# Performance work log

Hardware: AMD Instinct MI355X
Metric: run time of the kernel (lower is better)

## Reference

```python
import jax, jax.numpy as jnp
import numpy as np

NUM_CLASSES = 4      # config.class_num (malaria stages)
N = 2048             # total nodes = source + target samples
S = 1024             # source_length
FEAT_IN = 25088      # VGG19 include_top=False -> 7*7*512 flattened
D_FC = 512           # Dense(512)
D_G1 = 512           # config.features_dim (GCNConv1 out)
D_G2 = 256           # config.GCN_hidderlayer_dim_num (GCNConv2 out)


def setup_inputs() -> dict:
    key = jax.random.key(0)
    ks = jax.random.split(key, 8)
    sc = lambda fan_in: np.float32(1.0 / np.sqrt(fan_in))
    return {
        "x": jax.random.normal(ks[0], (N, FEAT_IN), jnp.float32),
        "W_fc": jax.random.normal(ks[1], (FEAT_IN, D_FC), jnp.float32) * sc(FEAT_IN),
        "b_fc": jnp.zeros((D_FC,), jnp.float32),
        "W_g1": jax.random.normal(ks[2], (D_FC, D_G1), jnp.float32) * sc(D_FC),
        "b_g1": jnp.zeros((D_G1,), jnp.float32),
        "W_g2": jax.random.normal(ks[3], (D_G1, D_G2), jnp.float32) * sc(D_G1),
        "b_g2": jnp.zeros((D_G2,), jnp.float32),
        "source_labels": jax.random.randint(ks[4], (S,), 0, NUM_CLASSES),
        "source_length": S,
    }


def reference(x, W_fc, b_fc, W_g1, b_g1, W_g2, b_g2, source_labels, source_length):
    # fc after (omitted frozen) VGG19 backbone + flatten
    feats = x @ W_fc + b_fc                                   # [N, 512]

    # get_centers: per-class SUM of source features (no averaging, faithful)
    src = feats[:source_length]                               # [S, 512]
    centers = jax.ops.segment_sum(src, source_labels, num_segments=NUM_CLASSES)  # [C, 512]

    # per-target euclidean distance to each centroid + argmin
    # (argmin of squared distance == argmin of euclidean distance)
    tgt = feats[source_length:]                               # [T, 512]
    d2 = (jnp.sum(tgt * tgt, axis=1, keepdims=True)
          - 2.0 * (tgt @ centers.T)
          + jnp.sum(centers * centers, axis=1)[None, :])      # [T, C]
    target_labels = jnp.argmin(d2, axis=1)                    # [T] int

    # label-cluster graph: edge iff same label; source block forced to identity
    all_labels = jnp.concatenate([source_labels.astype(jnp.int32),
                                  target_labels.astype(jnp.int32)])
    adj = (all_labels[:, None] == all_labels[None, :]).astype(feats.dtype)  # [N, N]
    adj = adj.at[:source_length, :source_length].set(
        jnp.eye(source_length, dtype=feats.dtype))

    # add_self_loops(value=1) then symmetric gcn_filter D^-1/2 A D^-1/2
    A = adj + jnp.eye(N, dtype=feats.dtype)
    dinv = jax.lax.rsqrt(jnp.sum(A, axis=1))                  # [N]
    A_norm = dinv[:, None] * A * dinv[None, :]                # [N, N]

    # two GCN layers (spektral GCNConv: A_norm @ (X @ W) + b) with relu
    h = jax.nn.relu(A_norm @ (feats @ W_g1) + b_g1)           # [N, 512]
    h = jax.nn.relu(A_norm @ (h @ W_g2) + b_g2)               # [N, 256]
    return (h, A_norm, feats)
```

## Files before the change

### kernel.cpp

```cpp
#include <hip/hip_runtime.h>

#define NROWS 2048
#define SLEN  1024
#define FEAT  25088
#define DFC   512
#define DG1   512
#define DG2   256
#define CSPLIT 128

typedef __attribute__((ext_vector_type(8))) short short8;
typedef __attribute__((ext_vector_type(4))) float f32x4;

__device__ __forceinline__ unsigned short bfbits(float f) {
  unsigned int u = __float_as_uint(f);
  u += 0x7fffu + ((u >> 16) & 1u);
  return (unsigned short)(u >> 16);
}

__device__ __forceinline__ unsigned int cvtpk(float lo, float hi) {
  unsigned int r;
  asm("v_cvt_pk_bf16_f32 %0, %1, %2" : "=v"(r) : "v"(lo), "v"(hi));
  return r;
}

__device__ __forceinline__ void load_lds16(const void* g, void* l) {
  __builtin_amdgcn_global_load_lds(
      (const __attribute__((address_space(1))) unsigned int*)g,
      (__attribute__((address_space(3))) unsigned int*)l, 16, 0, 0);
}

__global__ void transpose_cvt_k(const float* __restrict__ src, unsigned short* __restrict__ dst,
                                int K, int Ncol) {
  __shared__ float tile[64][65];
  int kb = blockIdx.x * 64, nb = blockIdx.y * 64;
  int tx = threadIdx.x & 63, ty = threadIdx.x >> 6;
  #pragma unroll
  for (int i = ty; i < 64; i += 4)
    tile[i][tx] = src[(size_t)(kb + i) * Ncol + (nb + tx)];
  __syncthreads();
  #pragma unroll
  for (int i = ty; i < 64; i += 4)
    dst[(size_t)(nb + i) * K + (kb + tx)] = bfbits(tile[tx][i]);
}

__global__ __launch_bounds__(512, 2) void gemm_fc_k(const float* __restrict__ A,
    const unsigned short* __restrict__ BT, float* __restrict__ Cacc, int ksteps) {
  __shared__ unsigned short Al[2][256 * 32];
  __shared__ unsigned short Bl[2][256 * 32];
  const int K = FEAT;
  int tid = threadIdx.x;
  int m0 = (blockIdx.x >> 1) * 256;
  int n0 = (blockIdx.x & 1) * 256;
  int kbase = blockIdx.y * ksteps * 32;
  int wid = tid >> 6, lane = tid & 63;
  int wm = wid >> 1, wn = wid & 1;
  int lrow = lane & 15, lko = lane >> 4;

  f32x4 acc[4][8];
  #pragma unroll
  for (int i = 0; i < 4; i++)
    #pragma unroll
    for (int j = 0; j < 8; j++) acc[i][j] = (f32x4){0.f, 0.f, 0.f, 0.f};

  float4 pa[4];

  auto loadA_regs = [&](int k0) {
    #pragma unroll
    for (int j = 0; j < 2; j++) {
      int ch = tid + j * 512;
      int r = ch >> 2, c = ch & 3;
      const float* g = A + (size_t)(m0 + r) * K + k0 + c * 8;
      pa[2 * j]     = *reinterpret_cast<const float4*>(g);
      pa[2 * j + 1] = *reinterpret_cast<const float4*>(g + 4);
    }
  };
  auto cvtWriteA = [&](int buf) {
    #pragma unroll
    for (int j = 0; j < 2; j++) {
      int ch = tid + j * 512;
      int r = ch >> 2, c = ch & 3;
      int p = c ^ (r & 3);
      int4 o;
      o.x = (int)cvtpk(pa[2 * j].x,     pa[2 * j].y);
      o.y = (int)cvtpk(pa[2 * j].z,     pa[2 * j].w);
      o.z = (int)cvtpk(pa[2 * j + 1].x, pa[2 * j + 1].y);
      o.w = (int)cvtpk(pa[2 * j + 1].z, pa[2 * j + 1].w);
      *reinterpret_cast<int4*>((char*)Al[buf] + r * 64 + p * 16) = o;
    }
  };
  auto stageB = [&](int buf, int k0) {
    #pragma unroll
    for (int j = 0; j < 2; j++) {
      int chb = wid * 128 + j * 64;
      int ch = chb + lane;
      int r = ch >> 2, c = (ch & 3) ^ (r & 3);
      load_lds16(BT + (size_t)(n0 + r) * K + k0 + c * 8, (char*)Bl[buf] + chb * 16);
    }
  };

  loadA_regs(kbase);
  stageB(0, kbase);
  cvtWriteA(0);
  loadA_regs(kbase + 32);
  stageB(1, kbase + 32);
  asm volatile("s_waitcnt vmcnt(6)" ::: "memory");
  asm volatile("s_waitcnt lgkmcnt(0)" ::: "memory");
  __builtin_amdgcn_s_barrier();
  __builtin_amdgcn_sched_barrier(0);

  int cur = 0;
  for (int t = 0; t < ksteps; ++t) {
    bool more1 = (t + 1 < ksteps), more2 = (t + 2 < ksteps);
    if (more1) cvtWriteA(cur ^ 1);
    short8 af[4], bf8[8];
    #pragma unroll
    for (int mi = 0; mi < 4; mi++) {
      int R = wm * 64 + mi * 16 + lrow;
      int p = lko ^ (R & 3);
      af[mi] = *reinterpret_cast<const short8*>((char*)Al[cur] + R * 64 + p * 16);
    }
    #pragma unroll
    for (int ni = 0; ni < 8; ni++) {
      int R = wn * 128 + ni * 16 + lrow;
      int p = lko ^ (R & 3);
      bf8[ni] = *reinterpret_cast<const short8*>((char*)Bl[cur] + R * 64 + p * 16);
    }
    if (more2) loadA_regs(kbase + (t + 2) * 32);
    asm volatile("s_waitcnt lgkmcnt(0)" ::: "memory");
    __builtin_amdgcn_s_barrier();
    __builtin_amdgcn_sched_barrier(0);
    if (more2) stageB(cur, kbase + (t + 2) * 32);
    #pragma unroll
    for (int mi = 0; mi < 4; mi++)
      #pragma unroll
      for (int ni = 0; ni < 8; ni++)
        acc[mi][ni] = __builtin_amdgcn_mfma_f32_16x16x32_bf16(af[mi], bf8[ni], acc[mi][ni], 0, 0, 0);
    if (more1) {
      if (more2) { asm volatile("s_waitcnt vmcnt(6)" ::: "memory"); }
      else       { asm volatile("s_waitcnt vmcnt(0)" ::: "memory"); }
      __builtin_amdgcn_sched_barrier(0);
    }
    cur ^= 1;
  }

  #pragma unroll
  for (int mi = 0; mi < 4; mi++)
    #pragma unroll
    for (int ni = 0; ni < 8; ni++)
      #pragma unroll
      for (int r = 0; r < 4; r++) {
        int row = m0 + wm * 64 + mi * 16 + lko * 4 + r;
        int col = n0 + wn * 128 + ni * 16 + lrow;
        atomicAdd(&Cacc[(size_t)row * DFC + col], acc[mi][ni][r]);
      }
}

__global__ __launch_bounds__(256) void gemm_l_k(const unsigned short* __restrict__ A,
    const unsigned short* __restrict__ BT, float* __restrict__ Cacc,
    int K, int Ncols, int tiles_n, int ksteps) {
  __shared__ unsigned short Al[2][128 * 64];
  __shared__ unsigned short Bl[2][128 * 64];
  int tid = threadIdx.x;
  int m0 = (blockIdx.x / tiles_n) * 128;
  int n0 = (blockIdx.x % tiles_n) * 128;
  int kbase = blockIdx.y * ksteps * 64;
  int wid = tid >> 6, lane = tid & 63;
  int wm = wid >> 1, wn = wid & 1;
  int lrow = lane & 15, lko = lane >> 4;

  f32x4 acc[4][4];
  #pragma unroll
  for (int i = 0; i < 4; i++)
    #pragma unroll
    for (int j = 0; j < 4; j++) acc[i][j] = (f32x4){0.f, 0.f, 0.f, 0.f};

  auto stage = [&](unsigned short (*L)[128 * 64], const unsigned short* G, int buf, int k0) {
    #pragma unroll
    for (int j = 0; j < 4; j++) {
      int chb = j * 256 + wid * 64;
      int ch = chb + lane;
      int r = ch >> 3, c = (ch & 7) ^ (r & 7);
      load_lds16(G + (size_t)r * K + k0 + c * 8, (char*)L[buf] + chb * 16);
    }
  };

  stage(Al, A + (size_t)m0 * K, 0, kbase);
  stage(Bl, BT + (size_t)n0 * K, 0, kbase);
  __syncthreads();

  int cur = 0;
  for (int t = 0; t < ksteps; ++t) {
    bool more = (t + 1 < ksteps);
    if (more) {
      stage(Al, A + (size_t)m0 * K, cur ^ 1, kbase + (t + 1) * 64);
      stage(Bl, BT + (size_t)n0 * K, cur ^ 1, kbase + (t + 1) * 64);
    }
    #pragma unroll
    for (int kk = 0; kk < 2; kk++) {
      short8 af[4], bfv[4];
      #pragma unroll
      for (int mi = 0; mi < 4; mi++) {
        int R = wm * 64 + mi * 16 + lrow;
        int slot = ((kk << 2) | lko) ^ (lrow & 7);
        af[mi] = *reinterpret_cast<const short8*>((char*)Al[cur] + R * 128 + slot * 16);
      }
      #pragma unroll
      for (int ni = 0; ni < 4; ni++) {
        int R = wn * 64 + ni * 16 + lrow;
        int slot = ((kk << 2) | lko) ^ (lrow & 7);
        bfv[ni] = *reinterpret_cast<const short8*>((char*)Bl[cur] + R * 128 + slot * 16);
      }
      #pragma unroll
      for (int mi = 0; mi < 4; mi++)
        #pragma unroll
        for (int ni = 0; ni < 4; ni++)
          acc[mi][ni] = __builtin_amdgcn_mfma_f32_16x16x32_bf16(af[mi], bfv[ni], acc[mi][ni], 0, 0, 0);
    }
    __syncthreads();
    cur ^= 1;
  }
  #pragma unroll
  for (int mi = 0; mi < 4; mi++)
    #pragma unroll
    for (int ni = 0; ni < 4; ni++)
      #pragma unroll
      for (int r = 0; r < 4; r++) {
        int row = m0 + wm * 64 + mi * 16 + lko * 4 + r;
        int col = n0 + wn * 64 + ni * 16 + lrow;
        atomicAdd(&Cacc[(size_t)row * Ncols + col], acc[mi][ni][r]);
      }
}

__global__ void feats_fin_k(const float* __restrict__ facc, const float* __restrict__ bfc,
                            float* __restrict__ outf, unsigned short* __restrict__ outbf) {
  int i = blockIdx.y;
  int n = blockIdx.x * 256 + threadIdx.x;
  float v = facc[(size_t)i * DFC + n] + bfc[n];
  outf[(size_t)i * DFC + n] = v;
  outbf[(size_t)i * DFC + n] = bfbits(v);
}

__global__ void seg_sum_part_k(const float* __restrict__ x, const int* __restrict__ slab,
                               float* __restrict__ sxp) {
  int k4 = blockIdx.x * 256 + threadIdx.x;
  if (k4 >= FEAT / 4) return;
  int k = k4 * 4;
  int i0 = blockIdx.y * 64, i1 = i0 + 64;
  float4 a0 = {0,0,0,0}, a1 = {0,0,0,0}, a2 = {0,0,0,0}, a3 = {0,0,0,0};
  #pragma unroll 4
  for (int i = i0; i < i1; i++) {
    float4 v = *reinterpret_cast<const float4*>(x + (size_t)i * FEAT + k);
    int c = slab[i];
    float m0 = (c == 0) ? 1.f : 0.f, m1 = (c == 1) ? 1.f : 0.f;
    float m2 = (c == 2) ? 1.f : 0.f, m3 = (c == 3) ? 1.f : 0.f;
    a0.x += m0 * v.x; a0.y += m0 * v.y; a0.z += m0 * v.z; a0.w += m0 * v.w;
    a1.x += m1 * v.x; a1.y += m1 * v.y; a1.z += m1 * v.z; a1.w += m1 * v.w;
    a2.x += m2 * v.x; a2.y += m2 * v.y; a2.z += m2 * v.z; a2.w += m2 * v.w;
    a3.x += m3 * v.x; a3.y += m3 * v.y; a3.z += m3 * v.z; a3.w += m3 * v.w;
  }
  size_t base = (size_t)blockIdx.y * 4 * FEAT;
  *reinterpret_cast<float4*>(sxp + base + 0 * FEAT + k) = a0;
  *reinterpret_cast<float4*>(sxp + base + 1 * FEAT + k) = a1;
  *reinterpret_cast<float4*>(sxp + base + 2 * FEAT + k) = a2;
  *reinterpret_cast<float4*>(sxp + base + 3 * FEAT + k) = a3;
}

__global__ void seg_sum_reduce_k(const float* __restrict__ sxp, float* __restrict__ sx) {
  int k4 = blockIdx.x * 256 + threadIdx.x;
  if (k4 >= FEAT / 4) return;
  int k = k4 * 4;
  int c = blockIdx.y;
  double s0 = 0, s1 = 0, s2 = 0, s3 = 0;
  #pragma unroll
  for (int p = 0; p < 16; p++) {
    float4 v = *reinterpret_cast<const float4*>(sxp + ((size_t)p * 4 + c) * FEAT + k);
    s0 += (double)v.x; s1 += (double)v.y; s2 += (double)v.z; s3 += (double)v.w;
  }
  float4 r; r.x = (float)s0; r.y = (float)s1; r.z = (float)s2; r.w = (float)s3;
  *reinterpret_cast<float4*>(sx + (size_t)c * FEAT + k) = r;
}

__global__ void count_src_k(const int* __restrict__ slab, int* __restrict__ cnt) {
  __shared__ int c[4];
  if (threadIdx.x < 4) c[threadIdx.x] = 0;
  __syncthreads();
  for (int i = threadIdx.x; i < SLEN; i += 256) atomicAdd(&c[slab[i]], 1);
  __syncthreads();
  if (threadIdx.x < 4) cnt[threadIdx.x] = c[threadIdx.x];
}

__global__ void centers_part_k(const float* __restrict__ sx, const float* __restrict__ W,
                               double* __restrict__ cpart) {
  int n = blockIdx.x * 64 + (threadIdx.x & 63);
  int cc = threadIdx.x >> 6;
  int kb = blockIdx.y * (FEAT / CSPLIT), ke = kb + FEAT / CSPLIT;
  const float* sr = sx + (size_t)cc * FEAT;
  double acc = 0.0;
  #pragma unroll 4
  for (int k = kb; k < ke; k++)
    acc += (double)sr[k] * (double)W[(size_t)k * DFC + n];
  cpart[((size_t)blockIdx.y * 4 + cc) * DFC + n] = acc;
}

__global__ void centers_reduce_k(const double* __restrict__ cpart, const float* __restrict__ bfc,
                                 const int* __restrict__ cntsrc, float* __restrict__ Cent) {
  int idx = blockIdx.x * 256 + threadIdx.x;
  int cc = idx >> 9, n = idx & 511;
  double s = 0.0;
  #pragma unroll 4
  for (int p = 0; p < CSPLIT; p++) s += cpart[((size_t)p * 4 + cc) * DFC + n];
  Cent[idx] = (float)(s + (double)cntsrc[cc] * (double)bfc[n]);
}

__global__ void wc_k(const float* __restrict__ W, const float* __restrict__ Cent,
                     float* __restrict__ wc) {
  __shared__ float cs[4 * DFC];
  for (int i = threadIdx.x; i < 4 * DFC; i += 256) cs[i] = Cent[i];
  __syncthreads();
  int k = blockIdx.x * 256 + threadIdx.x;
  if (k >= FEAT) return;
  const float* wr = W + (size_t)k * DFC;
  double a0 = 0, a1 = 0, a2 = 0, a3 = 0;
  #pragma unroll 2
  for (int n = 0; n < DFC; n += 4) {
    float4 w4 = *reinterpret_cast<const float4*>(wr + n);
    a0 += (double)w4.x * cs[0 * DFC + n] + (double)w4.y * cs[0 * DFC + n + 1]
        + (double)w4.z * cs[0 * DFC + n + 2] + (double)w4.w * cs[0 * DFC + n + 3];
    a1 += (double)w4.x * cs[1 * DFC + n] + (double)w4.y * cs[1 * DFC + n + 1]
        + (double)w4.z * cs[1 * DFC + n + 2] + (double)w4.w * cs[1 * DFC + n + 3];
    a2 += (double)w4.x * cs[2 * DFC + n] + (double)w4.y * cs[2 * DFC + n + 1]
        + (double)w4.z * cs[2 * DFC + n + 2] + (double)w4.w * cs[2 * DFC + n + 3];
    a3 += (double)w4.x * cs[3 * DFC + n] + (double)w4.y * cs[3 * DFC + n + 1]
        + (double)w4.z * cs[3 * DFC + n + 2] + (double)w4.w * cs[3 * DFC + n + 3];
  }
  float4 r; r.x = (float)a0; r.y = (float)a1; r.z = (float)a2; r.w = (float)a3;
  *reinterpret_cast<float4*>(wc + 4 * (size_t)k) = r;
}

__global__ void kj_k(const float* __restrict__ Cent, const float* __restrict__ bfc,
                     float* __restrict__ Kj) {
  int j = threadIdx.x >> 6, lane = threadIdx.x & 63;
  float cn = 0.f, bc = 0.f;
  for (int n = lane; n < DFC; n += 64) {
    float c = Cent[j * DFC + n];
    cn += c * c; bc += bfc[n] * c;
  }
  #pragma unroll
  for (int m = 32; m >= 1; m >>= 1) { cn += __shfl_xor(cn, m); bc += __shfl_xor(bc, m); }
  if (lane == 0) Kj[j] = cn - 2.f * bc;
}

__global__ void d2_labels_k(const float* __restrict__ x, const float* __restrict__ wc,
                            const float* __restrict__ Kj, int* __restrict__ tlab) {
  int row = blockIdx.x;
  int tid = threadIdx.x;
  const float* xr = x + (size_t)(SLEN + row) * FEAT;
  double a0 = 0, a1 = 0, a2 = 0, a3 = 0;
  #pragma unroll 2
  for (int k = tid; k < FEAT; k += 256) {
    float xv = xr[k];
    float4 w4 = *reinterpret_cast<const float4*>(wc + 4 * (size_t)k);
    a0 += (double)xv * w4.x; a1 += (double)xv * w4.y;
    a2 += (double)xv * w4.z; a3 += (double)xv * w4.w;
  }
  #pragma unroll
  for (int m = 32; m >= 1; m >>= 1) {
    a0 += __shfl_xor(a0, m); a1 += __shfl_xor(a1, m);
    a2 += __shfl_xor(a2, m); a3 += __shfl_xor(a3, m);
  }
  __shared__ double s[4][4];
  int wid = tid >> 6, lane = tid & 63;
  if (lane == 0) { s[wid][0] = a0; s[wid][1] = a1; s[wid][2] = a2; s[wid][3] = a3; }
  __syncthreads();
  if (tid == 0) {
    double t0 = s[0][0] + s[1][0] + s[2][0] + s[3][0];
    double t1 = s[0][1] + s[1][1] + s[2][1] + s[3][1];
    double t2 = s[0][2] + s[1][2] + s[2][2] + s[3][2];
    double t3 = s[0][3] + s[1][3] + s[2][3] + s[3][3];
    double s0 = (double)Kj[0] - 2.0 * t0;
    double s1 = (double)Kj[1] - 2.0 * t1;
    double s2 = (double)Kj[2] - 2.0 * t2;
    double s3 = (double)Kj[3] - 2.0 * t3;
    int bi = 0; double b = s0;
    if (s1 < b) { b = s1; bi = 1; }
    if (s2 < b) { b = s2; bi = 2; }
    if (s3 < b) { b = s3; bi = 3; }
    tlab[row] = bi;
  }
}

__global__ void finalize_labels_k(const int* __restrict__ slab, const int* __restrict__ tlab,
                                  const int* __restrict__ cntsrc, int* __restrict__ alllab,
                                  float* __restrict__ dinv) {
  __shared__ int ct[4];
  if (threadIdx.x < 4) ct[threadIdx.x] = 0;
  __syncthreads();
  for (int i = threadIdx.x; i < SLEN; i += 256) atomicAdd(&ct[tlab[i]], 1);
  __syncthreads();
  for (int i = threadIdx.x; i < NROWS; i += 256) {
    int lab = (i < SLEN) ? slab[i] : tlab[i - SLEN];
    alllab[i] = lab;
    float rs = (i < SLEN) ? (2.f + (float)ct[lab])
                          : (1.f + (float)cntsrc[lab] + (float)ct[lab]);
    dinv[i] = 1.f / sqrtf(rs);
  }
}

__global__ void anorm_k(const int* __restrict__ alllab, const float* __restrict__ dinv,
                        float* __restrict__ Aout) {
  int i = blockIdx.y;
  int j0 = (blockIdx.x * 256 + threadIdx.x) * 4;
  int li = alllab[i];
  float di = dinv[i];
  int4 lj = *reinterpret_cast<const int4*>(alllab + j0);
  float4 dj = *reinterpret_cast<const float4*>(dinv + j0);
  int jj[4] = {lj.x, lj.y, lj.z, lj.w};
  float dd[4] = {dj.x, dj.y, dj.z, dj.w};
  float4 o;
  float* op = &o.x;
  #pragma unroll
  for (int e = 0; e < 4; e++) {
    int j = j0 + e;
    float v;
    if (i == j) v = 2.f * di * dd[e];
    else if (i < SLEN && j < SLEN) v = 0.f;
    else v = (li == jj[e]) ? di * dd[e] : 0.f;
    op[e] = v;
  }
  *reinterpret_cast<float4*>(Aout + (size_t)i * NROWS + j0) = o;
}

__global__ void reduce_st_k(const float* __restrict__ Xacc, const int* __restrict__ alllab,
                            const float* __restrict__ dinv, float* __restrict__ ST, int D) {
  int n = blockIdx.x * 256 + threadIdx.x;
  int i0 = blockIdx.y * 32, i1 = i0 + 32;
  float s[4] = {0, 0, 0, 0}, tt[4] = {0, 0, 0, 0};
  for (int i = i0; i < i1; ++i) {
    float v = dinv[i] * Xacc[(size_t)i * D + n];
    int lab = alllab[i];
    bool src = i < SLEN;
    #pragma unroll
    for (int c = 0; c < 4; c++) {
      s[c]  += (src && lab == c) ? v : 0.f;
      tt[c] += (!src && lab == c) ? v : 0.f;
    }
  }
  #pragma unroll
  for (int c = 0; c < 4; c++) {
    atomicAdd(&ST[c * D + n], s[c]);
    atomicAdd(&ST[(4 + c) * D + n], tt[c]);
  }
}

__global__ void apply_prop_k(const float* __restrict__ Xacc, const float* __restrict__ ST,
                             const int* __restrict__ alllab, const float* __restrict__ dinv,
                             const float* __restrict__ bias, float* __restrict__ outf,
                             unsigned short* __restrict__ outbf, int D) {
  int i = blockIdx.y;
  int n = blockIdx.x * 256 + threadIdx.x;
  float dv = dinv[i];
  int lab = alllab[i];
  float xv = Xacc[(size_t)i * D + n];
  float z;
  if (i < SLEN) z = dv * (2.f * dv * xv + ST[(4 + lab) * D + n]);
  else          z = dv * (ST[lab * D + n] + ST[(4 + lab) * D + n] + dv * xv);
  z += bias[n];
  z = fmaxf(z, 0.f);
  if (outf)  outf[(size_t)i * D + n] = z;
  if (outbf) outbf[(size_t)i * D + n] = bfbits(z);
}

extern "C" void kernel_launch(void* const* d_in, const int* in_sizes, int n_in,
                              void* d_out, int out_size, void* d_ws, size_t ws_size,
                              hipStream_t stream) {
  const float* x    = (const float*)d_in[0];
  const float* Wfc  = (const float*)d_in[1];
  const float* bfc  = (const float*)d_in[2];
  const float* Wg1  = (const float*)d_in[3];
  const float* bg1  = (const float*)d_in[4];
  const float* Wg2  = (const float*)d_in[5];
  const float* bg2  = (const float*)d_in[6];
  const int*   slab = (const int*)d_in[7];

  float* out = (float*)d_out;
  float* out_h = out;
  float* out_A = out + 524288;
  float* out_f = out + 4718592;

  char* w = (char*)d_ws;
  unsigned short* wT   = (unsigned short*)(w);
  unsigned short* g1T  = (unsigned short*)(w + 25690112);
  unsigned short* g2T  = (unsigned short*)(w + 26214400);
  float* facc          = (float*)(w + 26476544);
  unsigned short* fbf  = (unsigned short*)(w + 30670848);
  float* x1acc         = (float*)(w + 32768000);
  unsigned short* h1bf = (unsigned short*)(w + 36962304);
  float* x2acc         = (float*)(w + 39059456);
  float* sx            = (float*)(w + 41156608);
  float* Cent          = (float*)(w + 41623552);
  float* wc            = (float*)(w + 41631744);
  float* Kj            = (float*)(w + 42033152);
  int*   tlab          = (int*)(w + 42033216);
  int*   alllab        = (int*)(w + 42037312);
  float* dinv          = (float*)(w + 42045504);
  int*   cntsrc        = (int*)(w + 42053696);
  float* ST1           = (float*)(w + 42053760);
  float* ST2           = (float*)(w + 42070144);

  float*  sxp     = (float*)(w + 32768000);
  double* cpart_d = (double*)(w + 39059456);

  hipMemsetAsync(facc,  0, (size_t)NROWS * DFC * 4, stream);
  hipMemsetAsync(ST1,   0, 8 * DG1 * 4, stream);
  hipMemsetAsync(ST2,   0, 8 * DG2 * 4, stream);

  transpose_cvt_k<<<dim3(FEAT / 64, DFC / 64), 256, 0, stream>>>(Wfc, wT, FEAT, DFC);
  transpose_cvt_k<<<dim3(DFC / 64, DG1 / 64), 256, 0, stream>>>(Wg1, g1T, DFC, DG1);
  transpose_cvt_k<<<dim3(DG1 / 64, DG2 / 64), 256, 0, stream>>>(Wg2, g2T, DG1, DG2);

  gemm_fc_k<<<dim3(16, 16), 512, 0, stream>>>(x, wT, facc, 49);
  feats_fin_k<<<dim3(DFC / 256, NROWS), 256, 0, stream>>>(facc, bfc, out_f, fbf);

  seg_sum_part_k<<<dim3(25, 16), 256, 0, stream>>>(x, slab, sxp);
  seg_sum_reduce_k<<<dim3(25, 4), 256, 0, stream>>>(sxp, sx);
  count_src_k<<<1, 256, 0, stream>>>(slab, cntsrc);
  centers_part_k<<<dim3(DFC / 64, CSPLIT), 256, 0, stream>>>(sx, Wfc, cpart_d);
  centers_reduce_k<<<dim3(4 * DFC / 256), 256, 0, stream>>>(cpart_d, bfc, cntsrc, Cent);
  wc_k<<<dim3(FEAT / 256), 256, 0, stream>>>(Wfc, Cent, wc);
  kj_k<<<1, 256, 0, stream>>>(Cent, bfc, Kj);
  d2_labels_k<<<dim3(NROWS - SLEN), 256, 0, stream>>>(x, wc, Kj, tlab);
  finalize_labels_k<<<1, 256, 0, stream>>>(slab, tlab, cntsrc, alllab, dinv);

  anorm_k<<<dim3(NROWS / 1024, NROWS), 256, 0, stream>>>(alllab, dinv, out_A);

  hipMemsetAsync(x1acc, 0, (size_t)NROWS * DG1 * 4, stream);
  gemm_l_k<<<dim3(16 * 4, 4), 256, 0, stream>>>(fbf, g1T, x1acc, DFC, DG1, 4, 2);
  reduce_st_k<<<dim3(DG1 / 256, 64), 256, 0, stream>>>(x1acc, alllab, dinv, ST1, DG1);
  apply_prop_k<<<dim3(DG1 / 256, NROWS), 256, 0, stream>>>(x1acc, ST1, alllab, dinv, bg1,
                                                           nullptr, h1bf, DG1);

  hipMemsetAsync(x2acc, 0, (size_t)NROWS * DG2 * 4, stream);
  gemm_l_k<<<dim3(16 * 2, 8), 256, 0, stream>>>(h1bf, g2T, x2acc, DG1, DG2, 2, 1);
  reduce_st_k<<<dim3(DG2 / 256, 64), 256, 0, stream>>>(x2acc, alllab, dinv, ST2, DG2);
  apply_prop_k<<<dim3(DG2 / 256, NROWS), 256, 0, stream>>>(x2acc, ST2, alllab, dinv, bg2,
                                                           out_h, nullptr, DG2);

  (void)in_sizes; (void)n_in; (void)out_size; (void)ws_size;
}
```

Baseline: 356.3 us.

## Triple-buffer LDS and deepen prefetch pipeline in FC GEMM

The fc GEMM kernel moves from double to triple buffering of the A and B LDS tiles. A and B loads are now issued three k-steps ahead, using two ping-pong register sets for the fp32 A prefetch, and the vmcnt waits are reworked to match. The LDS swizzle also changes to XOR with (row>>1)&3 to reduce bank conflicts. The aim is to hide more global-memory latency in this bandwidth-heavy 25088-deep reduction, at the cost of more LDS (96KB per block at 2 blocks/CU) and more registers, which may lower occupancy.

```diff
diff --git a/kernel.cpp b/kernel.cpp
--- a/kernel.cpp
+++ b/kernel.cpp
@@ -45,8 +45,8 @@
 
 __global__ __launch_bounds__(512, 2) void gemm_fc_k(const float* __restrict__ A,
     const unsigned short* __restrict__ BT, float* __restrict__ Cacc, int ksteps) {
-  __shared__ unsigned short Al[2][256 * 32];
-  __shared__ unsigned short Bl[2][256 * 32];
+  __shared__ unsigned short Al[3][256 * 32];
+  __shared__ unsigned short Bl[3][256 * 32];
   const int K = FEAT;
   int tid = threadIdx.x;
   int m0 = (blockIdx.x >> 1) * 256;
@@ -62,9 +62,9 @@
     #pragma unroll
     for (int j = 0; j < 8; j++) acc[i][j] = (f32x4){0.f, 0.f, 0.f, 0.f};
 
-  float4 pa[4];
-
-  auto loadA_regs = [&](int k0) {
+  float4 pa0[4], pa1[4];
+
+  auto loadA = [&](float4 (&pa)[4], int k0) {
     #pragma unroll
     for (int j = 0; j < 2; j++) {
       int ch = tid + j * 512;
@@ -74,73 +74,77 @@
       pa[2 * j + 1] = *reinterpret_cast<const float4*>(g + 4);
     }
   };
-  auto cvtWriteA = [&](int buf) {
+  auto cvtA = [&](float4 (&pa)[4], unsigned short* L) {
     #pragma unroll
     for (int j = 0; j < 2; j++) {
       int ch = tid + j * 512;
       int r = ch >> 2, c = ch & 3;
-      int p = c ^ (r & 3);
+      int p = c ^ ((r >> 1) & 3);
       int4 o;
       o.x = (int)cvtpk(pa[2 * j].x,     pa[2 * j].y);
       o.y = (int)cvtpk(pa[2 * j].z,     pa[2 * j].w);
       o.z = (int)cvtpk(pa[2 * j + 1].x, pa[2 * j + 1].y);
       o.w = (int)cvtpk(pa[2 * j + 1].z, pa[2 * j + 1].w);
-      *reinterpret_cast<int4*>((char*)Al[buf] + r * 64 + p * 16) = o;
+      *reinterpret_cast<int4*>((char*)L + r * 64 + p * 16) = o;
     }
   };
-  auto stageB = [&](int buf, int k0) {
+  auto stB = [&](unsigned short* L, int k0) {
     #pragma unroll
     for (int j = 0; j < 2; j++) {
       int chb = wid * 128 + j * 64;
       int ch = chb + lane;
-      int r = ch >> 2, c = (ch & 3) ^ (r & 3);
-      load_lds16(BT + (size_t)(n0 + r) * K + k0 + c * 8, (char*)Bl[buf] + chb * 16);
+      int r = ch >> 2, p = ch & 3;
+      int c = p ^ ((r >> 1) & 3);
+      load_lds16(BT + (size_t)(n0 + r) * K + k0 + c * 8, (char*)L + chb * 16);
     }
   };
 
-  loadA_regs(kbase);
-  stageB(0, kbase);
-  cvtWriteA(0);
-  loadA_regs(kbase + 32);
-  stageB(1, kbase + 32);
-  asm volatile("s_waitcnt vmcnt(6)" ::: "memory");
+  stB(Bl[0], kbase);
+  loadA(pa0, kbase);
+  loadA(pa1, kbase + 32);
+  cvtA(pa0, Al[0]);
+  stB(Bl[1], kbase + 32);
+  loadA(pa0, kbase + 64);
+  stB(Bl[2], kbase + 64);
   asm volatile("s_waitcnt lgkmcnt(0)" ::: "memory");
   __builtin_amdgcn_s_barrier();
   __builtin_amdgcn_sched_barrier(0);
 
   int cur = 0;
-  for (int t = 0; t < ksteps; ++t) {
-    bool more1 = (t + 1 < ksteps), more2 = (t + 2 < ksteps);
-    if (more1) cvtWriteA(cur ^ 1);
+  auto step = [&](int t, float4 (&pa)[4]) {
+    int nxt = (cur == 2) ? 0 : cur + 1;
+    if (t + 1 < ksteps) cvtA(pa, Al[nxt]);
     short8 af[4], bf8[8];
     #pragma unroll
     for (int mi = 0; mi < 4; mi++) {
       int R = wm * 64 + mi * 16 + lrow;
-      int p = lko ^ (R & 3);
+      int p = lko ^ ((R >> 1) & 3);
       af[mi] = *reinterpret_cast<const short8*>((char*)Al[cur] + R * 64 + p * 16);
     }
     #pragma unroll
     for (int ni = 0; ni < 8; ni++) {
       int R = wn * 128 + ni * 16 + lrow;
-      int p = lko ^ (R & 3);
+      int p = lko ^ ((R >> 1) & 3);
       bf8[ni] = *reinterpret_cast<const short8*>((char*)Bl[cur] + R * 64 + p * 16);
     }
-    if (more2) loadA_regs(kbase + (t + 2) * 32);
+    if (t + 3 < ksteps) loadA(pa, kbase + (t + 3) * 32);
+    if (t < ksteps - 4) { asm volatile("s_waitcnt vmcnt(10)" ::: "memory"); }
+    else                { asm volatile("s_waitcnt vmcnt(0)"  ::: "memory"); }
     asm volatile("s_waitcnt lgkmcnt(0)" ::: "memory");
     __builtin_amdgcn_s_barrier();
     __builtin_amdgcn_sched_barrier(0);
-    if (more2) stageB(cur, kbase + (t + 2) * 32);
+    if (t + 3 < ksteps) stB(Bl[cur], kbase + (t + 3) * 32);
     #pragma unroll
     for (int mi = 0; mi < 4; mi++)
       #pragma unroll
       for (int ni = 0; ni < 8; ni++)
         acc[mi][ni] = __builtin_amdgcn_mfma_f32_16x16x32_bf16(af[mi], bf8[ni], acc[mi][ni], 0, 0, 0);
-    if (more1) {
-      if (more2) { asm volatile("s_waitcnt vmcnt(6)" ::: "memory"); }
-      else       { asm volatile("s_waitcnt vmcnt(0)" ::: "memory"); }
-      __builtin_amdgcn_sched_barrier(0);
-    }
-    cur ^= 1;
+    cur = nxt;
+  };
+
+  for (int t0 = 0; t0 < ksteps; t0 += 2) {
+    step(t0, pa1);
+    if (t0 + 1 < ksteps) step(t0 + 1, pa0);
   }
 
   #pragma unroll
```

Result: no change. 357.6 us (+0.4%).

## Shrink fc GEMM tiles to 128x128 with simple single-buffered loop

Applied to the files above, without the earlier changes.

Replaces the 256x256-tile, 512-thread, register-prefetched double-buffered fc GEMM with a 128x128-tile, 256-thread kernel that loads, converts and stages each k-step synchronously. This raises block count and allows more blocks per CU so occupancy can hide latency instead of explicit pipelining. It also changes the LDS swizzle pattern. The trade-off is that the fp32 input matrix is re-read twice as often and prefetch overlap is lost.

```diff
diff --git a/kernel.cpp b/kernel.cpp
--- a/kernel.cpp
+++ b/kernel.cpp
@@ -43,114 +43,81 @@
     dst[(size_t)(nb + i) * K + (kb + tx)] = bfbits(tile[tx][i]);
 }
 
-__global__ __launch_bounds__(512, 2) void gemm_fc_k(const float* __restrict__ A,
+__global__ __launch_bounds__(256, 4) void gemm_fc_k(const float* __restrict__ A,
     const unsigned short* __restrict__ BT, float* __restrict__ Cacc, int ksteps) {
-  __shared__ unsigned short Al[2][256 * 32];
-  __shared__ unsigned short Bl[2][256 * 32];
+  __shared__ unsigned short Al[128 * 32];
+  __shared__ unsigned short Bl[128 * 32];
   const int K = FEAT;
   int tid = threadIdx.x;
-  int m0 = (blockIdx.x >> 1) * 256;
-  int n0 = (blockIdx.x & 1) * 256;
+  int m0 = (blockIdx.x >> 2) * 128;
+  int n0 = (blockIdx.x & 3) * 128;
   int kbase = blockIdx.y * ksteps * 32;
   int wid = tid >> 6, lane = tid & 63;
   int wm = wid >> 1, wn = wid & 1;
   int lrow = lane & 15, lko = lane >> 4;
 
-  f32x4 acc[4][8];
+  int chA0 = tid, rA0 = chA0 >> 2, cA0 = chA0 & 3, pA0 = cA0 ^ ((rA0 >> 1) & 3);
+  int chA1 = tid + 256, rA1 = chA1 >> 2, cA1 = chA1 & 3, pA1 = cA1 ^ ((rA1 >> 1) & 3);
+  int chB0 = wid * 128 + lane;
+  int chB1 = wid * 128 + 64 + lane;
+  int rB0 = chB0 >> 2, cB0 = (chB0 & 3) ^ ((rB0 >> 1) & 3);
+  int rB1 = chB1 >> 2, cB1 = (chB1 & 3) ^ ((rB1 >> 1) & 3);
+  const float* gA0 = A + (size_t)(m0 + rA0) * K + cA0 * 8;
+  const float* gA1 = A + (size_t)(m0 + rA1) * K + cA1 * 8;
+  const unsigned short* gB0 = BT + (size_t)(n0 + rB0) * K + cB0 * 8;
+  const unsigned short* gB1 = BT + (size_t)(n0 + rB1) * K + cB1 * 8;
+
+  f32x4 acc[4][4];
   #pragma unroll
   for (int i = 0; i < 4; i++)
     #pragma unroll
-    for (int j = 0; j < 8; j++) acc[i][j] = (f32x4){0.f, 0.f, 0.f, 0.f};
-
-  float4 pa[4];
-
-  auto loadA_regs = [&](int k0) {
-    #pragma unroll
-    for (int j = 0; j < 2; j++) {
-      int ch = tid + j * 512;
-      int r = ch >> 2, c = ch & 3;
-      const float* g = A + (size_t)(m0 + r) * K + k0 + c * 8;
-      pa[2 * j]     = *reinterpret_cast<const float4*>(g);
-      pa[2 * j + 1] = *reinterpret_cast<const float4*>(g + 4);
-    }
-  };
-  auto cvtWriteA = [&](int buf) {
-    #pragma unroll
-    for (int j = 0; j < 2; j++) {
-      int ch = tid + j * 512;
-      int r = ch >> 2, c = ch & 3;
-      int p = c ^ (r & 3);
-      int4 o;
-      o.x = (int)cvtpk(pa[2 * j].x,     pa[2 * j].y);
-      o.y = (int)cvtpk(pa[2 * j].z,     pa[2 * j].w);
-      o.z = (int)cvtpk(pa[2 * j + 1].x, pa[2 * j + 1].y);
-      o.w = (int)cvtpk(pa[2 * j + 1].z, pa[2 * j + 1].w);
-      *reinterpret_cast<int4*>((char*)Al[buf] + r * 64 + p * 16) = o;
-    }
-  };
-  auto stageB = [&](int buf, int k0) {
-    #pragma unroll
-    for (int j = 0; j < 2; j++) {
-      int chb = wid * 128 + j * 64;
-      int ch = chb + lane;
-      int r = ch >> 2, c = (ch & 3) ^ (r & 3);
-      load_lds16(BT + (size_t)(n0 + r) * K + k0 + c * 8, (char*)Bl[buf] + chb * 16);
-    }
-  };
-
-  loadA_regs(kbase);
-  stageB(0, kbase);
-  cvtWriteA(0);
-  loadA_regs(kbase + 32);
-  stageB(1, kbase + 32);
-  asm volatile("s_waitcnt vmcnt(6)" ::: "memory");
-  asm volatile("s_waitcnt lgkmcnt(0)" ::: "memory");
-  __builtin_amdgcn_s_barrier();
-  __builtin_amdgcn_sched_barrier(0);
-
-  int cur = 0;
+    for (int j = 0; j < 4; j++) acc[i][j] = (f32x4){0.f, 0.f, 0.f, 0.f};
+
   for (int t = 0; t < ksteps; ++t) {
-    bool more1 = (t + 1 < ksteps), more2 = (t + 2 < ksteps);
-    if (more1) cvtWriteA(cur ^ 1);
-    short8 af[4], bf8[8];
+    int k0 = kbase + t * 32;
+    float4 v00 = *reinterpret_cast<const float4*>(gA0 + k0);
+    float4 v01 = *reinterpret_cast<const float4*>(gA0 + k0 + 4);
+    float4 v10 = *reinterpret_cast<const float4*>(gA1 + k0);
+    float4 v11 = *reinterpret_cast<const float4*>(gA1 + k0 + 4);
+    int4 o0, o1;
+    o0.x = (int)cvtpk(v00.x, v00.y); o0.y = (int)cvtpk(v00.z, v00.w);
+    o0.z = (int)cvtpk(v01.x, v01.y); o0.w = (int)cvtpk(v01.z, v01.w);
+    o1.x = (int)cvtpk(v10.x, v10.y); o1.y = (int)cvtpk(v10.z, v10.w);
+    o1.z = (int)cvtpk(v11.x, v11.y); o1.w = (int)cvtpk(v11.z, v11.w);
+    __syncthreads();
+    *reinterpret_cast<int4*>((char*)Al + rA0 * 64 + pA0 * 16) = o0;
+    *reinterpret_cast<int4*>((char*)Al + rA1 * 64 + pA1 * 16) = o1;
+    load_lds16(gB0 + k0, (char*)Bl + chB0 * 16);
+    load_lds16(gB1 + k0, (char*)Bl + chB1 * 16);
+    __syncthreads();
+    short8 af[4], bfv[4];
     #pragma unroll
     for (int mi = 0; mi < 4; mi++) {
       int R = wm * 64 + mi * 16 + lrow;
-      int p = lko ^ (R & 3);
-      af[mi] = *reinterpret_cast<const short8*>((char*)Al[cur] + R * 64 + p * 16);
+      int p = lko ^ ((R >> 1) & 3);
+      af[mi] = *reinterpret_cast<const short8*>((char*)Al + R * 64 + p * 16);
     }
     #pragma unroll
-    for (int ni = 0; ni < 8; ni++) {
-      int R = wn * 128 + ni * 16 + lrow;
-      int p = lko ^ (R & 3);
-      bf8[ni] = *reinterpret_cast<const short8*>((char*)Bl[cur] + R * 64 + p * 16);
+    for (int ni = 0; ni < 4; ni++) {
+      int R = wn * 64 + ni * 16 + lrow;
+      int p = lko ^ ((R >> 1) & 3);
+      bfv[ni] = *reinterpret_cast<const short8*>((char*)Bl + R * 64 + p * 16);
     }
-    if (more2) loadA_regs(kbase + (t + 2) * 32);
-    asm volatile("s_waitcnt lgkmcnt(0)" ::: "memory");
-    __builtin_amdgcn_s_barrier();
-    __builtin_amdgcn_sched_barrier(0);
-    if (more2) stageB(cur, kbase + (t + 2) * 32);
     #pragma unroll
     for (int mi = 0; mi < 4; mi++)
       #pragma unroll
-      for (int ni = 0; ni < 8; ni++)
-        acc[mi][ni] = __builtin_amdgcn_mfma_f32_16x16x32_bf16(af[mi], bf8[ni], acc[mi][ni], 0, 0, 0);
-    if (more1) {
-      if (more2) { asm volatile("s_waitcnt vmcnt(6)" ::: "memory"); }
-      else       { asm volatile("s_waitcnt vmcnt(0)" ::: "memory"); }
-      __builtin_amdgcn_sched_barrier(0);
-    }
-    cur ^= 1;
+      for (int ni = 0; ni < 4; ni++)
+        acc[mi][ni] = __builtin_amdgcn_mfma_f32_16x16x32_bf16(af[mi], bfv[ni], acc[mi][ni], 0, 0, 0);
   }
 
   #pragma unroll
   for (int mi = 0; mi < 4; mi++)
     #pragma unroll
-    for (int ni = 0; ni < 8; ni++)
+    for (int ni = 0; ni < 4; ni++)
       #pragma unroll
       for (int r = 0; r < 4; r++) {
         int row = m0 + wm * 64 + mi * 16 + lko * 4 + r;
-        int col = n0 + wn * 128 + ni * 16 + lrow;
+        int col = n0 + wn * 64 + ni * 16 + lrow;
         atomicAdd(&Cacc[(size_t)row * DFC + col], acc[mi][ni][r]);
       }
 }
@@ -518,7 +485,7 @@
   transpose_cvt_k<<<dim3(DFC / 64, DG1 / 64), 256, 0, stream>>>(Wg1, g1T, DFC, DG1);
   transpose_cvt_k<<<dim3(DG1 / 64, DG2 / 64), 256, 0, stream>>>(Wg2, g2T, DG1, DG2);
 
-  gemm_fc_k<<<dim3(16, 16), 512, 0, stream>>>(x, wT, facc, 49);
+  gemm_fc_k<<<dim3(64, 16), 256, 0, stream>>>(x, wT, facc, 49);
   feats_fin_k<<<dim3(DFC / 256, NROWS), 256, 0, stream>>>(facc, bfc, out_f, fbf);
 
   seg_sum_part_k<<<dim3(25, 16), 256, 0, stream>>>(x, slab, sxp);
```

After: 393.6 us. 10.4% more time.
